# Kernel tuning notes

Hardware: AMD Instinct MI355X
Metric: run time of the kernel (lower is better)

The kernel has to match this reference:

```python
import jax, jax.numpy as jnp
import numpy as np

N_ACTIONS = 4
HIDDEN = 32

def setup_inputs() -> dict:
    key = jax.random.key(0)
    ks = jax.random.split(key, 8)
    B, T = 2048, 1024
    prev_actions_onehot = jax.random.uniform(ks[0], (B, T, N_ACTIONS), dtype=jnp.float32)
    prev_rewards = jax.random.normal(ks[1], (B, T, 1), dtype=jnp.float32)
    in_dim = N_ACTIONS + 1
    s_ih = 1.0 / np.sqrt(HIDDEN)
    W_ih = jax.random.uniform(ks[2], (HIDDEN, in_dim), jnp.float32, -s_ih, s_ih)
    W_hh = jax.random.uniform(ks[3], (HIDDEN, HIDDEN), jnp.float32, -s_ih, s_ih)
    b_ih = jax.random.uniform(ks[4], (HIDDEN,), jnp.float32, -s_ih, s_ih)
    b_hh = jax.random.uniform(ks[5], (HIDDEN,), jnp.float32, -s_ih, s_ih)
    W_ro = jax.random.uniform(ks[6], (N_ACTIONS, HIDDEN), jnp.float32, -s_ih, s_ih)
    b_ro = jax.random.uniform(ks[7], (N_ACTIONS,), jnp.float32, -s_ih, s_ih)
    return {
        'prev_actions_onehot': prev_actions_onehot,
        'prev_rewards': prev_rewards,
        'W_ih': W_ih, 'W_hh': W_hh, 'b_ih': b_ih, 'b_hh': b_hh,
        'W_ro': W_ro, 'b_ro': b_ro,
    }

def reference(prev_actions_onehot, prev_rewards, W_ih, W_hh, b_ih, b_hh, W_ro, b_ro):
    # x_seq: [B, T, n_actions+1]
    x_seq = jnp.concatenate([prev_actions_onehot, prev_rewards], axis=-1)
    B = x_seq.shape[0]
    # Precompute the input projection for all steps (parallel): [B, T, H]
    x_proj = jnp.einsum('bti,hi->bth', x_seq, W_ih) + b_ih + b_hh
    h0 = jnp.zeros((B, HIDDEN), dtype=x_seq.dtype)

    def step(h, xp_t):
        # xp_t: [B, H] (already contains x@W_ih^T + b_ih + b_hh)
        h_new = jnp.tanh(xp_t + h @ W_hh.T)
        return h_new, h_new

    # scan over time: move T to leading axis
    h_T, hs = jax.lax.scan(step, h0, jnp.swapaxes(x_proj, 0, 1))
    hs = jnp.swapaxes(hs, 0, 1)  # [B, T, H]
    logits_seq = jnp.einsum('bth,ah->bta', hs, W_ro) + b_ro  # [B, T, n_actions]
    return logits_seq, h_T
```

## Files before the change

kernel.cpp:

```cpp
#include <hip/hip_runtime.h>

#define H 32
#define GPB 8

__device__ __forceinline__ float fast_tanh(float x) {
    float e = __builtin_amdgcn_exp2f(x * 2.8853900817779268f);
    float r = __builtin_amdgcn_rcpf(e + 1.0f);
    return fmaf(-2.0f, r, 1.0f);
}

__global__ __launch_bounds__(256, 1) void rnn_fused(
    const float* __restrict__ onehot,
    const float* __restrict__ rewards,
    const float* __restrict__ W_ih,
    const float* __restrict__ W_hh,
    const float* __restrict__ b_ih,
    const float* __restrict__ b_hh,
    const float* __restrict__ W_ro,
    const float* __restrict__ b_ro,
    float* __restrict__ out_logits,
    float* __restrict__ out_hT,
    int T)
{
    const int tid = threadIdx.x;
    const int j = tid & 31;
    const int g = tid >> 5;
    const int b = blockIdx.x * GPB + g;

    __shared__ __align__(16) float hx[GPB][36];

    float whh[H];
#pragma unroll
    for (int k = 0; k < 8; ++k) {
        float4 w = *(const float4*)(W_hh + j * H + 4 * k);
        whh[4*k+0] = w.x; whh[4*k+1] = w.y; whh[4*k+2] = w.z; whh[4*k+3] = w.w;
    }
    const int a = j & 3;
    float wro[H];
#pragma unroll
    for (int k = 0; k < 8; ++k) {
        float4 w = *(const float4*)(W_ro + a * H + 4 * k);
        wro[4*k+0] = w.x; wro[4*k+1] = w.y; wro[4*k+2] = w.z; wro[4*k+3] = w.w;
    }
    const float wih0 = W_ih[j*5+0], wih1 = W_ih[j*5+1], wih2 = W_ih[j*5+2],
                wih3 = W_ih[j*5+3], wih4 = W_ih[j*5+4];
    const float bias = b_ih[j] + b_hh[j];
    const float bro  = b_ro[a];

    const float* oh_ptr = onehot  + (size_t)b * T * 4;
    const float* rw_ptr = rewards + (size_t)b * T;
    float*       lg_ptr = out_logits + (size_t)b * T * 4;

    float4 oh0 = *(const float4*)(oh_ptr + 0);
    float4 oh1 = *(const float4*)(oh_ptr + 4);
    float4 oh2 = *(const float4*)(oh_ptr + 8);
    float4 oh3 = *(const float4*)(oh_ptr + 12);
    float4 rw  = *(const float4*)(rw_ptr);

    float hj = 0.0f;
    float hA[H], hB[H];

    auto readout = [&](const float (&hv)[H], int t) {
        float l0 = 0.f, l1 = 0.f, l2 = 0.f, l3 = 0.f;
#pragma unroll
        for (int k = 0; k < 8; ++k) {
            l0 = fmaf(hv[4*k+0], wro[4*k+0], l0);
            l1 = fmaf(hv[4*k+1], wro[4*k+1], l1);
            l2 = fmaf(hv[4*k+2], wro[4*k+2], l2);
            l3 = fmaf(hv[4*k+3], wro[4*k+3], l3);
        }
        float lg = ((l0 + l1) + (l2 + l3)) + bro;
        if (j < 4) lg_ptr[(size_t)t * 4 + j] = lg;
    };

    auto step = [&](float (&cur)[H], const float (&prv)[H], float xp, int t) {
        hx[g][j] = hj;
#pragma unroll
        for (int k = 0; k < 8; ++k) {
            float4 v = *(const float4*)(&hx[g][4 * k]);
            cur[4*k+0] = v.x; cur[4*k+1] = v.y;
            cur[4*k+2] = v.z; cur[4*k+3] = v.w;
        }
        if (t >= 2) readout(prv, t - 2);
        float a0 = xp, a1 = 0.f, a2 = 0.f, a3 = 0.f;
#pragma unroll
        for (int k = 0; k < 8; ++k) {
            a0 = fmaf(cur[4*k+0], whh[4*k+0], a0);
            a1 = fmaf(cur[4*k+1], whh[4*k+1], a1);
            a2 = fmaf(cur[4*k+2], whh[4*k+2], a2);
            a3 = fmaf(cur[4*k+3], whh[4*k+3], a3);
        }
        hj = fast_tanh((a0 + a1) + (a2 + a3));
    };

    for (int tb = 0; tb < T; tb += 4) {
        float xp0 = fmaf(oh0.x,wih0, fmaf(oh0.y,wih1, fmaf(oh0.z,wih2, fmaf(oh0.w,wih3, fmaf(rw.x,wih4, bias)))));
        float xp1 = fmaf(oh1.x,wih0, fmaf(oh1.y,wih1, fmaf(oh1.z,wih2, fmaf(oh1.w,wih3, fmaf(rw.y,wih4, bias)))));
        float xp2 = fmaf(oh2.x,wih0, fmaf(oh2.y,wih1, fmaf(oh2.z,wih2, fmaf(oh2.w,wih3, fmaf(rw.z,wih4, bias)))));
        float xp3 = fmaf(oh3.x,wih0, fmaf(oh3.y,wih1, fmaf(oh3.z,wih2, fmaf(oh3.w,wih3, fmaf(rw.w,wih4, bias)))));

        if (tb + 4 < T) {
            oh0 = *(const float4*)(oh_ptr + (size_t)(tb + 4) * 4);
            oh1 = *(const float4*)(oh_ptr + (size_t)(tb + 5) * 4);
            oh2 = *(const float4*)(oh_ptr + (size_t)(tb + 6) * 4);
            oh3 = *(const float4*)(oh_ptr + (size_t)(tb + 7) * 4);
            rw  = *(const float4*)(rw_ptr + tb + 4);
        }

        step(hA, hB, xp0, tb + 0);
        step(hB, hA, xp1, tb + 1);
        step(hA, hB, xp2, tb + 2);
        step(hB, hA, xp3, tb + 3);
    }

    readout(hB, T - 2);
    hx[g][j] = hj;
#pragma unroll
    for (int k = 0; k < 8; ++k) {
        float4 v = *(const float4*)(&hx[g][4 * k]);
        hA[4*k+0] = v.x; hA[4*k+1] = v.y; hA[4*k+2] = v.z; hA[4*k+3] = v.w;
    }
    readout(hA, T - 1);
    out_hT[(size_t)b * H + j] = hj;
}

extern "C" void kernel_launch(void* const* d_in, const int* in_sizes, int n_in,
                              void* d_out, int out_size, void* d_ws, size_t ws_size,
                              hipStream_t stream) {
    const float* onehot  = (const float*)d_in[0];
    const float* rewards = (const float*)d_in[1];
    const float* W_ih    = (const float*)d_in[2];
    const float* W_hh    = (const float*)d_in[3];
    const float* b_ih    = (const float*)d_in[4];
    const float* b_hh    = (const float*)d_in[5];
    const float* W_ro    = (const float*)d_in[6];
    const float* b_ro    = (const float*)d_in[7];

    const int T = 1024;
    const int B = in_sizes[1] / T;

    float* out_logits = (float*)d_out;
    float* out_hT     = (float*)d_out + (size_t)B * T * 4;

    dim3 block(256);
    dim3 grid(B / GPB);
    rnn_fused<<<grid, block, 0, stream>>>(onehot, rewards, W_ih, W_hh,
                                          b_ih, b_hh, W_ro, b_ro,
                                          out_logits, out_hT, T);
}
```

Measured before the change: 362.3 us.

## Distribute hidden state across lane quads and use DPP FMAs for recurrence

Each lane now reads only 8 of the 32 hidden values from LDS (two float4s instead of eight). The full 32-element dot product is formed with v_fmac_f32_dpp quad_perm broadcasts that pull the other lanes' slices. The readout is spread across lanes: each lane computes a 4-term partial sum, the partials are reduced with DPP row shifts, and one lane per group of 8 writes the logit. The first iteration is peeled to drop the per-step t>=2 check. This cuts LDS read traffic and register pressure on the serial critical path, but relies on inline asm DPP semantics and on the lane-mapping being correct.

```diff
diff --git a/kernel.cpp b/kernel.cpp
--- a/kernel.cpp
+++ b/kernel.cpp
@@ -2,12 +2,29 @@
 
 #define H 32
 #define GPB 8
+#define PITCH 48
 
 __device__ __forceinline__ float fast_tanh(float x) {
     float e = __builtin_amdgcn_exp2f(x * 2.8853900817779268f);
     float r = __builtin_amdgcn_rcpf(e + 1.0f);
     return fmaf(-2.0f, r, 1.0f);
 }
+
+#define QFMA(acc, p, w, q) \
+    asm("v_fmac_f32_dpp %0, %1, %2 quad_perm:[" #q "," #q "," #q "," #q "] row_mask:0xf bank_mask:0xf" \
+        : "+v"(acc) : "v"(p), "v"(w))
+
+#define CH8(acc, q) \
+    QFMA(acc, pN[0], whh[8*q+0], q); QFMA(acc, pN[1], whh[8*q+1], q); \
+    QFMA(acc, pN[2], whh[8*q+2], q); QFMA(acc, pN[3], whh[8*q+3], q); \
+    QFMA(acc, pN[4], whh[8*q+4], q); QFMA(acc, pN[5], whh[8*q+5], q); \
+    QFMA(acc, pN[6], whh[8*q+6], q); QFMA(acc, pN[7], whh[8*q+7], q)
+
+#define DPPMOV(x, ctrl) \
+    __int_as_float(__builtin_amdgcn_update_dpp(0, __float_as_int(x), (ctrl), 0xf, 0xf, true))
+#define ROW_SHR1 0x111
+#define ROW_SHR2 0x112
+#define ROW_SHR4 0x114
 
 __global__ __launch_bounds__(256, 1) void rnn_fused(
     const float* __restrict__ onehot,
@@ -23,11 +40,18 @@
     int T)
 {
     const int tid = threadIdx.x;
-    const int j = tid & 31;
-    const int g = tid >> 5;
-    const int b = blockIdx.x * GPB + g;
+    const int j   = tid & 31;
+    const int g   = tid >> 5;
+    const int b   = blockIdx.x * GPB + g;
+    const int qp  = j & 3;
+    const int r   = j >> 3;
+    const bool hi = ((j >> 2) & 1) != 0;
+    const bool writer = (j & 7) == 7;
 
-    __shared__ __align__(16) float hx[GPB][36];
+    __shared__ __align__(16) float hx[GPB * PITCH];
+    float* lds_wr = &hx[g * PITCH + j];
+    const float4* lds_rd0 = (const float4*)&hx[g * PITCH + qp * 8];
+    const float4* lds_rd1 = lds_rd0 + 1;
 
     float whh[H];
 #pragma unroll
@@ -35,17 +59,11 @@
         float4 w = *(const float4*)(W_hh + j * H + 4 * k);
         whh[4*k+0] = w.x; whh[4*k+1] = w.y; whh[4*k+2] = w.z; whh[4*k+3] = w.w;
     }
-    const int a = j & 3;
-    float wro[H];
-#pragma unroll
-    for (int k = 0; k < 8; ++k) {
-        float4 w = *(const float4*)(W_ro + a * H + 4 * k);
-        wro[4*k+0] = w.x; wro[4*k+1] = w.y; wro[4*k+2] = w.z; wro[4*k+3] = w.w;
-    }
     const float wih0 = W_ih[j*5+0], wih1 = W_ih[j*5+1], wih2 = W_ih[j*5+2],
                 wih3 = W_ih[j*5+3], wih4 = W_ih[j*5+4];
     const float bias = b_ih[j] + b_hh[j];
-    const float bro  = b_ro[a];
+    const float4 wr4 = *(const float4*)(W_ro + r * H + qp * 8 + (hi ? 4 : 0));
+    const float bro = b_ro[r];
 
     const float* oh_ptr = onehot  + (size_t)b * T * 4;
     const float* rw_ptr = rewards + (size_t)b * T;
@@ -58,47 +76,56 @@
     float4 rw  = *(const float4*)(rw_ptr);
 
     float hj = 0.0f;
-    float hA[H], hB[H];
+    float pA[8], pB[8];
 
-    auto readout = [&](const float (&hv)[H], int t) {
-        float l0 = 0.f, l1 = 0.f, l2 = 0.f, l3 = 0.f;
-#pragma unroll
-        for (int k = 0; k < 8; ++k) {
-            l0 = fmaf(hv[4*k+0], wro[4*k+0], l0);
-            l1 = fmaf(hv[4*k+1], wro[4*k+1], l1);
-            l2 = fmaf(hv[4*k+2], wro[4*k+2], l2);
-            l3 = fmaf(hv[4*k+3], wro[4*k+3], l3);
-        }
-        float lg = ((l0 + l1) + (l2 + l3)) + bro;
-        if (j < 4) lg_ptr[(size_t)t * 4 + j] = lg;
+    auto readout = [&](const float (&p)[8], int t) {
+        float s0 = hi ? p[4] : p[0];
+        float s1 = hi ? p[5] : p[1];
+        float s2 = hi ? p[6] : p[2];
+        float s3 = hi ? p[7] : p[3];
+        float s = fmaf(s3, wr4.w, fmaf(s2, wr4.z, fmaf(s1, wr4.y, s0 * wr4.x)));
+        s += DPPMOV(s, ROW_SHR1);
+        s += DPPMOV(s, ROW_SHR2);
+        s += DPPMOV(s, ROW_SHR4);
+        if (writer) lg_ptr[(size_t)t * 4 + r] = s + bro;
     };
 
-    auto step = [&](float (&cur)[H], const float (&prv)[H], float xp, int t) {
-        hx[g][j] = hj;
-#pragma unroll
-        for (int k = 0; k < 8; ++k) {
-            float4 v = *(const float4*)(&hx[g][4 * k]);
-            cur[4*k+0] = v.x; cur[4*k+1] = v.y;
-            cur[4*k+2] = v.z; cur[4*k+3] = v.w;
-        }
-        if (t >= 2) readout(prv, t - 2);
+    auto step = [&](float (&pN)[8], const float (&pO)[8], float xp, int t, bool ro) {
+        *lds_wr = hj;
+        float4 v0 = *lds_rd0;
+        float4 v1 = *lds_rd1;
+        pN[0]=v0.x; pN[1]=v0.y; pN[2]=v0.z; pN[3]=v0.w;
+        pN[4]=v1.x; pN[5]=v1.y; pN[6]=v1.z; pN[7]=v1.w;
+        if (ro) readout(pO, t - 2);
         float a0 = xp, a1 = 0.f, a2 = 0.f, a3 = 0.f;
-#pragma unroll
-        for (int k = 0; k < 8; ++k) {
-            a0 = fmaf(cur[4*k+0], whh[4*k+0], a0);
-            a1 = fmaf(cur[4*k+1], whh[4*k+1], a1);
-            a2 = fmaf(cur[4*k+2], whh[4*k+2], a2);
-            a3 = fmaf(cur[4*k+3], whh[4*k+3], a3);
-        }
+        CH8(a0, 0);
+        CH8(a1, 1);
+        CH8(a2, 2);
+        CH8(a3, 3);
         hj = fast_tanh((a0 + a1) + (a2 + a3));
     };
 
-    for (int tb = 0; tb < T; tb += 4) {
+    {
         float xp0 = fmaf(oh0.x,wih0, fmaf(oh0.y,wih1, fmaf(oh0.z,wih2, fmaf(oh0.w,wih3, fmaf(rw.x,wih4, bias)))));
         float xp1 = fmaf(oh1.x,wih0, fmaf(oh1.y,wih1, fmaf(oh1.z,wih2, fmaf(oh1.w,wih3, fmaf(rw.y,wih4, bias)))));
         float xp2 = fmaf(oh2.x,wih0, fmaf(oh2.y,wih1, fmaf(oh2.z,wih2, fmaf(oh2.w,wih3, fmaf(rw.z,wih4, bias)))));
         float xp3 = fmaf(oh3.x,wih0, fmaf(oh3.y,wih1, fmaf(oh3.z,wih2, fmaf(oh3.w,wih3, fmaf(rw.w,wih4, bias)))));
+        oh0 = *(const float4*)(oh_ptr + 16);
+        oh1 = *(const float4*)(oh_ptr + 20);
+        oh2 = *(const float4*)(oh_ptr + 24);
+        oh3 = *(const float4*)(oh_ptr + 28);
+        rw  = *(const float4*)(rw_ptr + 4);
+        step(pA, pB, xp0, 0, false);
+        step(pB, pA, xp1, 1, false);
+        step(pA, pB, xp2, 2, true);
+        step(pB, pA, xp3, 3, true);
+    }
 
+    for (int tb = 4; tb < T; tb += 4) {
+        float xp0 = fmaf(oh0.x,wih0, fmaf(oh0.y,wih1, fmaf(oh0.z,wih2, fmaf(oh0.w,wih3, fmaf(rw.x,wih4, bias)))));
+        float xp1 = fmaf(oh1.x,wih0, fmaf(oh1.y,wih1, fmaf(oh1.z,wih2, fmaf(oh1.w,wih3, fmaf(rw.y,wih4, bias)))));
+        float xp2 = fmaf(oh2.x,wih0, fmaf(oh2.y,wih1, fmaf(oh2.z,wih2, fmaf(oh2.w,wih3, fmaf(rw.z,wih4, bias)))));
+        float xp3 = fmaf(oh3.x,wih0, fmaf(oh3.y,wih1, fmaf(oh3.z,wih2, fmaf(oh3.w,wih3, fmaf(rw.w,wih4, bias)))));
         if (tb + 4 < T) {
             oh0 = *(const float4*)(oh_ptr + (size_t)(tb + 4) * 4);
             oh1 = *(const float4*)(oh_ptr + (size_t)(tb + 5) * 4);
@@ -106,22 +133,23 @@
             oh3 = *(const float4*)(oh_ptr + (size_t)(tb + 7) * 4);
             rw  = *(const float4*)(rw_ptr + tb + 4);
         }
-
-        step(hA, hB, xp0, tb + 0);
-        step(hB, hA, xp1, tb + 1);
-        step(hA, hB, xp2, tb + 2);
-        step(hB, hA, xp3, tb + 3);
+        step(pA, pB, xp0, tb + 0, true);
+        step(pB, pA, xp1, tb + 1, true);
+        step(pA, pB, xp2, tb + 2, true);
+        step(pB, pA, xp3, tb + 3, true);
     }
 
-    readout(hB, T - 2);
-    hx[g][j] = hj;
-#pragma unroll
-    for (int k = 0; k < 8; ++k) {
-        float4 v = *(const float4*)(&hx[g][4 * k]);
-        hA[4*k+0] = v.x; hA[4*k+1] = v.y; hA[4*k+2] = v.z; hA[4*k+3] = v.w;
+    readout(pB, T - 2);
+    *lds_wr = hj;
+    {
+        float4 v0 = *lds_rd0;
+        float4 v1 = *lds_rd1;
+        pA[0]=v0.x; pA[1]=v0.y; pA[2]=v0.z; pA[3]=v0.w;
+        pA[4]=v1.x; pA[5]=v1.y; pA[6]=v1.z; pA[7]=v1.w;
     }
-    readout(hA, T - 1);
+    readout(pA, T - 1);
     out_hT[(size_t)b * H + j] = hj;
+
 }
 
 extern "C" void kernel_launch(void* const* d_in, const int* in_sizes, int n_in,
```

Measured after the change: 322.2 us. 11.1% less time.

## Replace LDS hidden-state broadcast with DPP row rotations and swizzle

Applied to the files above, without the earlier changes.

The per-step shared-memory write and read-back of the hidden vector is replaced by in-register exchange. Each step uses 15 DPP row-rotate ops within 16-lane rows plus one ds_swizzle across the two halves of the 32-lane group. The W_hh and W_ro weights are pre-permuted per lane to match the rotation order. The readout is fused into the same rotation pass, so logits for t-1 come out with the recurrence FMAs, and the explicit hA/hB arrays go away. The risk is that the recurrence now waits on a serial chain of DPP ops each step, and this relies on the DPP row semantics being correct for wave64.

```diff
diff --git a/kernel.cpp b/kernel.cpp
--- a/kernel.cpp
+++ b/kernel.cpp
@@ -8,6 +8,24 @@
     float r = __builtin_amdgcn_rcpf(e + 1.0f);
     return fmaf(-2.0f, r, 1.0f);
 }
+
+template<int K>
+__device__ __forceinline__ float rorK(float v) {
+    return __int_as_float(__builtin_amdgcn_update_dpp(
+        __float_as_int(v), __float_as_int(v), 0x120 | K, 0xf, 0xf, false));
+}
+
+#define PHK(K, V, W, R) { float tK = rorK<K>(V); \
+    aAcc[K & 1] = fmaf(tK, W[K], aAcc[K & 1]); \
+    rAcc[K & 1] = fmaf(tK, R[K], rAcc[K & 1]); }
+
+#define PHASE(V, W, R) \
+    aAcc[0] = fmaf(V, W[0], aAcc[0]); rAcc[0] = fmaf(V, R[0], rAcc[0]); \
+    PHK(1,V,W,R)  PHK(2,V,W,R)  PHK(3,V,W,R)  PHK(4,V,W,R)  PHK(5,V,W,R) \
+    PHK(6,V,W,R)  PHK(7,V,W,R)  PHK(8,V,W,R)  PHK(9,V,W,R)  PHK(10,V,W,R) \
+    PHK(11,V,W,R) PHK(12,V,W,R) PHK(13,V,W,R) PHK(14,V,W,R) PHK(15,V,W,R)
+
+#define SWIZ_XOR16 0x401F
 
 __global__ __launch_bounds__(256, 1) void rnn_fused(
     const float* __restrict__ onehot,
@@ -23,28 +41,25 @@
     int T)
 {
     const int tid = threadIdx.x;
-    const int j = tid & 31;
+    const int u = tid & 31;
     const int g = tid >> 5;
     const int b = blockIdx.x * GPB + g;
+    const int i = u & 15;
+    const int r = u >> 4;
+    const int a = u & 3;
 
-    __shared__ __align__(16) float hx[GPB][36];
-
-    float whh[H];
+    float wA[16], wB[16], roA[16], roB[16];
 #pragma unroll
-    for (int k = 0; k < 8; ++k) {
-        float4 w = *(const float4*)(W_hh + j * H + 4 * k);
-        whh[4*k+0] = w.x; whh[4*k+1] = w.y; whh[4*k+2] = w.z; whh[4*k+3] = w.w;
+    for (int k = 0; k < 16; ++k) {
+        int col = (i - k) & 15;
+        wA[k]  = W_hh[u * H + 16 * r       + col];
+        wB[k]  = W_hh[u * H + 16 * (1 - r) + col];
+        roA[k] = W_ro[a * H + 16 * r       + col];
+        roB[k] = W_ro[a * H + 16 * (1 - r) + col];
     }
-    const int a = j & 3;
-    float wro[H];
-#pragma unroll
-    for (int k = 0; k < 8; ++k) {
-        float4 w = *(const float4*)(W_ro + a * H + 4 * k);
-        wro[4*k+0] = w.x; wro[4*k+1] = w.y; wro[4*k+2] = w.z; wro[4*k+3] = w.w;
-    }
-    const float wih0 = W_ih[j*5+0], wih1 = W_ih[j*5+1], wih2 = W_ih[j*5+2],
-                wih3 = W_ih[j*5+3], wih4 = W_ih[j*5+4];
-    const float bias = b_ih[j] + b_hh[j];
+    const float wih0 = W_ih[u*5+0], wih1 = W_ih[u*5+1], wih2 = W_ih[u*5+2],
+                wih3 = W_ih[u*5+3], wih4 = W_ih[u*5+4];
+    const float bias = b_ih[u] + b_hh[u];
     const float bro  = b_ro[a];
 
     const float* oh_ptr = onehot  + (size_t)b * T * 4;
@@ -58,47 +73,40 @@
     float4 rw  = *(const float4*)(rw_ptr);
 
     float hj = 0.0f;
-    float hA[H], hB[H];
 
-    auto readout = [&](const float (&hv)[H], int t) {
-        float l0 = 0.f, l1 = 0.f, l2 = 0.f, l3 = 0.f;
-#pragma unroll
-        for (int k = 0; k < 8; ++k) {
-            l0 = fmaf(hv[4*k+0], wro[4*k+0], l0);
-            l1 = fmaf(hv[4*k+1], wro[4*k+1], l1);
-            l2 = fmaf(hv[4*k+2], wro[4*k+2], l2);
-            l3 = fmaf(hv[4*k+3], wro[4*k+3], l3);
-        }
-        float lg = ((l0 + l1) + (l2 + l3)) + bro;
-        if (j < 4) lg_ptr[(size_t)t * 4 + j] = lg;
+    auto step = [&](float xp, int tm1, bool wr) {
+        int mi = __builtin_amdgcn_ds_swizzle(__float_as_int(hj), SWIZ_XOR16);
+        float aAcc[2] = {xp, 0.f};
+        float rAcc[2] = {0.f, 0.f};
+        PHASE(hj, wA, roA);
+        float m = __int_as_float(mi);
+        PHASE(m, wB, roB);
+        hj = fast_tanh(aAcc[0] + aAcc[1]);
+        if (wr && u < 4)
+            lg_ptr[(size_t)tm1 * 4 + u] = (rAcc[0] + rAcc[1]) + bro;
     };
 
-    auto step = [&](float (&cur)[H], const float (&prv)[H], float xp, int t) {
-        hx[g][j] = hj;
-#pragma unroll
-        for (int k = 0; k < 8; ++k) {
-            float4 v = *(const float4*)(&hx[g][4 * k]);
-            cur[4*k+0] = v.x; cur[4*k+1] = v.y;
-            cur[4*k+2] = v.z; cur[4*k+3] = v.w;
-        }
-        if (t >= 2) readout(prv, t - 2);
-        float a0 = xp, a1 = 0.f, a2 = 0.f, a3 = 0.f;
-#pragma unroll
-        for (int k = 0; k < 8; ++k) {
-            a0 = fmaf(cur[4*k+0], whh[4*k+0], a0);
-            a1 = fmaf(cur[4*k+1], whh[4*k+1], a1);
-            a2 = fmaf(cur[4*k+2], whh[4*k+2], a2);
-            a3 = fmaf(cur[4*k+3], whh[4*k+3], a3);
-        }
-        hj = fast_tanh((a0 + a1) + (a2 + a3));
-    };
-
-    for (int tb = 0; tb < T; tb += 4) {
+    {
         float xp0 = fmaf(oh0.x,wih0, fmaf(oh0.y,wih1, fmaf(oh0.z,wih2, fmaf(oh0.w,wih3, fmaf(rw.x,wih4, bias)))));
         float xp1 = fmaf(oh1.x,wih0, fmaf(oh1.y,wih1, fmaf(oh1.z,wih2, fmaf(oh1.w,wih3, fmaf(rw.y,wih4, bias)))));
         float xp2 = fmaf(oh2.x,wih0, fmaf(oh2.y,wih1, fmaf(oh2.z,wih2, fmaf(oh2.w,wih3, fmaf(rw.z,wih4, bias)))));
         float xp3 = fmaf(oh3.x,wih0, fmaf(oh3.y,wih1, fmaf(oh3.z,wih2, fmaf(oh3.w,wih3, fmaf(rw.w,wih4, bias)))));
+        oh0 = *(const float4*)(oh_ptr + 16);
+        oh1 = *(const float4*)(oh_ptr + 20);
+        oh2 = *(const float4*)(oh_ptr + 24);
+        oh3 = *(const float4*)(oh_ptr + 28);
+        rw  = *(const float4*)(rw_ptr + 4);
+        step(xp0, -1, false);
+        step(xp1,  0, true);
+        step(xp2,  1, true);
+        step(xp3,  2, true);
+    }
 
+    for (int tb = 4; tb < T; tb += 4) {
+        float xp0 = fmaf(oh0.x,wih0, fmaf(oh0.y,wih1, fmaf(oh0.z,wih2, fmaf(oh0.w,wih3, fmaf(rw.x,wih4, bias)))));
+        float xp1 = fmaf(oh1.x,wih0, fmaf(oh1.y,wih1, fmaf(oh1.z,wih2, fmaf(oh1.w,wih3, fmaf(rw.y,wih4, bias)))));
+        float xp2 = fmaf(oh2.x,wih0, fmaf(oh2.y,wih1, fmaf(oh2.z,wih2, fmaf(oh2.w,wih3, fmaf(rw.z,wih4, bias)))));
+        float xp3 = fmaf(oh3.x,wih0, fmaf(oh3.y,wih1, fmaf(oh3.z,wih2, fmaf(oh3.w,wih3, fmaf(rw.w,wih4, bias)))));
         if (tb + 4 < T) {
             oh0 = *(const float4*)(oh_ptr + (size_t)(tb + 4) * 4);
             oh1 = *(const float4*)(oh_ptr + (size_t)(tb + 5) * 4);
@@ -106,22 +114,25 @@
             oh3 = *(const float4*)(oh_ptr + (size_t)(tb + 7) * 4);
             rw  = *(const float4*)(rw_ptr + tb + 4);
         }
-
-        step(hA, hB, xp0, tb + 0);
-        step(hB, hA, xp1, tb + 1);
-        step(hA, hB, xp2, tb + 2);
-        step(hB, hA, xp3, tb + 3);
+        step(xp0, tb - 1, true);
+        step(xp1, tb + 0, true);
+        step(xp2, tb + 1, true);
+        step(xp3, tb + 2, true);
     }
 
-    readout(hB, T - 2);
-    hx[g][j] = hj;
-#pragma unroll
-    for (int k = 0; k < 8; ++k) {
-        float4 v = *(const float4*)(&hx[g][4 * k]);
-        hA[4*k+0] = v.x; hA[4*k+1] = v.y; hA[4*k+2] = v.z; hA[4*k+3] = v.w;
+    {
+        int mi = __builtin_amdgcn_ds_swizzle(__float_as_int(hj), SWIZ_XOR16);
+        float aAcc[2] = {0.f, 0.f};
+        float rAcc[2] = {0.f, 0.f};
+        PHASE(hj, wA, roA);
+        float m = __int_as_float(mi);
+        PHASE(m, wB, roB);
+        (void)aAcc;
+        if (u < 4)
+            lg_ptr[(size_t)(T - 1) * 4 + u] = (rAcc[0] + rAcc[1]) + bro;
     }
-    readout(hA, T - 1);
-    out_hT[(size_t)b * H + j] = hj;
+    out_hT[(size_t)b * H + u] = hj;
+
 }
 
 extern "C" void kernel_launch(void* const* d_in, const int* in_sizes, int n_in,
```

New measurement: 393.8 us. 8.7% more time.

## Split hidden matvec across half-waves with DPP FMAs and bpermute broadcasts, interleaving two sequences

Applied to the files above, without the earlier changes.

Each 64-lane wave now handles two batch sequences. For each sequence, the K dimension of the W_hh matvec is split across the two 32-lane halves and the partial sums are exchanged with ds_bpermute. The hidden state is stored as the sigmoid-form r = 1/(1+e^{2y}), with tanh = 1 - 2r folded into the weights (-2*W) and constant terms (rsum, roconst). The h broadcast uses bpermute plus DPP quad_perm FMAs instead of LDS stores and loads. The readout uses DPP row shifts for its reduction, and interleaving the two independent recurrences is meant to hide dependency latency, at the cost of more cross-lane traffic and reliance on inline assembly.

```diff
diff --git a/kernel.cpp b/kernel.cpp
--- a/kernel.cpp
+++ b/kernel.cpp
@@ -1,13 +1,22 @@
 #include <hip/hip_runtime.h>
 
-#define H 32
-#define GPB 8
-
-__device__ __forceinline__ float fast_tanh(float x) {
-    float e = __builtin_amdgcn_exp2f(x * 2.8853900817779268f);
-    float r = __builtin_amdgcn_rcpf(e + 1.0f);
-    return fmaf(-2.0f, r, 1.0f);
-}
+#define KK 2.8853900817779268f
+
+#define QFMA(acc, p, w, q) \
+    asm("v_fmac_f32_dpp %0, %1, %2 quad_perm:[" #q "," #q "," #q "," #q "] row_mask:0xf bank_mask:0xf" \
+        : "+v"(acc) : "v"(p), "v"(w))
+
+#define Q4(acc, p, w2, q) \
+    QFMA(acc, p[0], w2[4*q+0], q); QFMA(acc, p[1], w2[4*q+1], q); \
+    QFMA(acc, p[2], w2[4*q+2], q); QFMA(acc, p[3], w2[4*q+3], q)
+
+#define DPPMOV(x, ctrl) \
+    __int_as_float(__builtin_amdgcn_update_dpp(0, __float_as_int(x), (ctrl), 0xf, 0xf, true))
+#define ROW_SHR1 0x111
+#define ROW_SHR2 0x112
+#define ROW_SHR4 0x114
+
+#define BPERM(idx, v) __builtin_amdgcn_ds_bpermute((idx), (v))
 
 __global__ __launch_bounds__(256, 1) void rnn_fused(
     const float* __restrict__ onehot,
@@ -22,106 +31,178 @@
     float* __restrict__ out_hT,
     int T)
 {
-    const int tid = threadIdx.x;
-    const int j = tid & 31;
-    const int g = tid >> 5;
-    const int b = blockIdx.x * GPB + g;
-
-    __shared__ __align__(16) float hx[GPB][36];
-
-    float whh[H];
+    const int tid  = threadIdx.x;
+    const int l    = tid & 63;
+    const int wv   = tid >> 6;
+    const int s    = l >> 5;
+    const int u    = l & 31;
+    const int qp   = l & 3;
+    const int ridx = u >> 3;
+    const bool oddq = ((u >> 2) & 1) != 0;
+    const bool writer = (l < 32) && ((u & 7) == 7);
+
+    const int bA = blockIdx.x * 8 + 2 * wv;
+    const int bB = bA + 1;
+
+    const int gib = (48 * s + 4 * qp) << 2;
+    const int lx  = (l ^ 32) << 2;
+
+    float w2[16];
+    float rsum = 0.f;
 #pragma unroll
-    for (int k = 0; k < 8; ++k) {
-        float4 w = *(const float4*)(W_hh + j * H + 4 * k);
-        whh[4*k+0] = w.x; whh[4*k+1] = w.y; whh[4*k+2] = w.z; whh[4*k+3] = w.w;
-    }
-    const int a = j & 3;
-    float wro[H];
+    for (int k4 = 0; k4 < 4; ++k4) {
+        float4 wq = *(const float4*)(W_hh + u * 32 + 16 * s + 4 * k4);
+        rsum += (wq.x + wq.y) + (wq.z + wq.w);
+        w2[4*k4+0] = -2.f * wq.x; w2[4*k4+1] = -2.f * wq.y;
+        w2[4*k4+2] = -2.f * wq.z; w2[4*k4+3] = -2.f * wq.w;
+    }
+    const float wih0 = W_ih[u*5+0], wih1 = W_ih[u*5+1], wih2 = W_ih[u*5+2],
+                wih3 = W_ih[u*5+3], wih4 = W_ih[u*5+4];
+    const float bias = b_ih[u] + b_hh[u];
+
+    float wro2[4];
+    {
+        float4 wq = *(const float4*)(W_ro + ridx * 32 + 16 * s + 4 * qp);
+        wro2[0] = oddq ? 0.f : -2.f * wq.x;
+        wro2[1] = oddq ? 0.f : -2.f * wq.y;
+        wro2[2] = oddq ? 0.f : -2.f * wq.z;
+        wro2[3] = oddq ? 0.f : -2.f * wq.w;
+    }
+    float roconst = b_ro[ridx];
 #pragma unroll
-    for (int k = 0; k < 8; ++k) {
-        float4 w = *(const float4*)(W_ro + a * H + 4 * k);
-        wro[4*k+0] = w.x; wro[4*k+1] = w.y; wro[4*k+2] = w.z; wro[4*k+3] = w.w;
-    }
-    const float wih0 = W_ih[j*5+0], wih1 = W_ih[j*5+1], wih2 = W_ih[j*5+2],
-                wih3 = W_ih[j*5+3], wih4 = W_ih[j*5+4];
-    const float bias = b_ih[j] + b_hh[j];
-    const float bro  = b_ro[a];
-
-    const float* oh_ptr = onehot  + (size_t)b * T * 4;
-    const float* rw_ptr = rewards + (size_t)b * T;
-    float*       lg_ptr = out_logits + (size_t)b * T * 4;
-
-    float4 oh0 = *(const float4*)(oh_ptr + 0);
-    float4 oh1 = *(const float4*)(oh_ptr + 4);
-    float4 oh2 = *(const float4*)(oh_ptr + 8);
-    float4 oh3 = *(const float4*)(oh_ptr + 12);
-    float4 rw  = *(const float4*)(rw_ptr);
-
-    float hj = 0.0f;
-    float hA[H], hB[H];
-
-    auto readout = [&](const float (&hv)[H], int t) {
-        float l0 = 0.f, l1 = 0.f, l2 = 0.f, l3 = 0.f;
-#pragma unroll
-        for (int k = 0; k < 8; ++k) {
-            l0 = fmaf(hv[4*k+0], wro[4*k+0], l0);
-            l1 = fmaf(hv[4*k+1], wro[4*k+1], l1);
-            l2 = fmaf(hv[4*k+2], wro[4*k+2], l2);
-            l3 = fmaf(hv[4*k+3], wro[4*k+3], l3);
-        }
-        float lg = ((l0 + l1) + (l2 + l3)) + bro;
-        if (j < 4) lg_ptr[(size_t)t * 4 + j] = lg;
+    for (int k4 = 0; k4 < 8; ++k4) {
+        float4 t4 = *(const float4*)(W_ro + ridx * 32 + 4 * k4);
+        roconst += (t4.x + t4.y) + (t4.z + t4.w);
+    }
+
+    const float* ohpA = onehot  + (size_t)bA * T * 4;
+    const float* ohpB = onehot  + (size_t)bB * T * 4;
+    const float* rwpA = rewards + (size_t)bA * T;
+    const float* rwpB = rewards + (size_t)bB * T;
+    float*       lgpA = out_logits + (size_t)bA * T * 4;
+    float*       lgpB = out_logits + (size_t)bB * T * 4;
+
+    float4 A0 = *(const float4*)(ohpA + 0), A1 = *(const float4*)(ohpA + 4);
+    float4 A2 = *(const float4*)(ohpA + 8), A3 = *(const float4*)(ohpA + 12);
+    float4 Ar = *(const float4*)(rwpA);
+    float4 B0 = *(const float4*)(ohpB + 0), B1 = *(const float4*)(ohpB + 4);
+    float4 B2 = *(const float4*)(ohpB + 8), B3 = *(const float4*)(ohpB + 12);
+    float4 Br = *(const float4*)(rwpB);
+
+    float rA = 0.5f, rB = 0.5f;
+    float pA[4] = {0.5f, 0.5f, 0.5f, 0.5f};
+    float pB[4] = {0.5f, 0.5f, 0.5f, 0.5f};
+
+    auto macro = [&](float xa, float xb, int tm1, bool ro) {
+        float xaE = s ? 0.f : xa;
+        float xbE = s ? 0.f : xb;
+        float a0 = xaE + rsum, a1 = 0.f;
+        Q4(a0, pA, w2, 0); Q4(a0, pA, w2, 1);
+        Q4(a1, pA, w2, 2); Q4(a1, pA, w2, 3);
+        float partA = a0 + a1;
+        int XA = BPERM(lx, __float_as_int(partA));
+        float rpA = fmaf(pA[3], wro2[3], fmaf(pA[2], wro2[2],
+                    fmaf(pA[1], wro2[1], pA[0] * wro2[0])));
+        rpA += DPPMOV(rpA, ROW_SHR1);
+        rpA += DPPMOV(rpA, ROW_SHR2);
+        rpA += DPPMOV(rpA, ROW_SHR4);
+        int XRA = BPERM(lx, __float_as_int(rpA));
+        float b0 = xbE + rsum, b1 = 0.f;
+        Q4(b0, pB, w2, 0); Q4(b0, pB, w2, 1);
+        Q4(b1, pB, w2, 2); Q4(b1, pB, w2, 3);
+        float partB = b0 + b1;
+        int XB = BPERM(lx, __float_as_int(partB));
+        float rpB = fmaf(pB[3], wro2[3], fmaf(pB[2], wro2[2],
+                    fmaf(pB[1], wro2[1], pB[0] * wro2[0])));
+        rpB += DPPMOV(rpB, ROW_SHR1);
+        rpB += DPPMOV(rpB, ROW_SHR2);
+        rpB += DPPMOV(rpB, ROW_SHR4);
+        int XRB = BPERM(lx, __float_as_int(rpB));
+        float yA = partA + __int_as_float(XA);
+        rA = __builtin_amdgcn_rcpf(__builtin_amdgcn_exp2f(KK * yA) + 1.0f);
+        {
+            int hb = __float_as_int(rA);
+            pA[0] = __int_as_float(BPERM(gib +  0, hb));
+            pA[1] = __int_as_float(BPERM(gib +  4, hb));
+            pA[2] = __int_as_float(BPERM(gib +  8, hb));
+            pA[3] = __int_as_float(BPERM(gib + 12, hb));
+        }
+        if (ro && writer)
+            lgpA[(size_t)tm1 * 4 + ridx] = (rpA + __int_as_float(XRA)) + roconst;
+        float yB = partB + __int_as_float(XB);
+        rB = __builtin_amdgcn_rcpf(__builtin_amdgcn_exp2f(KK * yB) + 1.0f);
+        {
+            int hb = __float_as_int(rB);
+            pB[0] = __int_as_float(BPERM(gib +  0, hb));
+            pB[1] = __int_as_float(BPERM(gib +  4, hb));
+            pB[2] = __int_as_float(BPERM(gib +  8, hb));
+            pB[3] = __int_as_float(BPERM(gib + 12, hb));
+        }
+        if (ro && writer)
+            lgpB[(size_t)tm1 * 4 + ridx] = (rpB + __int_as_float(XRB)) + roconst;
     };
 
-    auto step = [&](float (&cur)[H], const float (&prv)[H], float xp, int t) {
-        hx[g][j] = hj;
-#pragma unroll
-        for (int k = 0; k < 8; ++k) {
-            float4 v = *(const float4*)(&hx[g][4 * k]);
-            cur[4*k+0] = v.x; cur[4*k+1] = v.y;
-            cur[4*k+2] = v.z; cur[4*k+3] = v.w;
-        }
-        if (t >= 2) readout(prv, t - 2);
-        float a0 = xp, a1 = 0.f, a2 = 0.f, a3 = 0.f;
-#pragma unroll
-        for (int k = 0; k < 8; ++k) {
-            a0 = fmaf(cur[4*k+0], whh[4*k+0], a0);
-            a1 = fmaf(cur[4*k+1], whh[4*k+1], a1);
-            a2 = fmaf(cur[4*k+2], whh[4*k+2], a2);
-            a3 = fmaf(cur[4*k+3], whh[4*k+3], a3);
-        }
-        hj = fast_tanh((a0 + a1) + (a2 + a3));
-    };
-
-    for (int tb = 0; tb < T; tb += 4) {
-        float xp0 = fmaf(oh0.x,wih0, fmaf(oh0.y,wih1, fmaf(oh0.z,wih2, fmaf(oh0.w,wih3, fmaf(rw.x,wih4, bias)))));
-        float xp1 = fmaf(oh1.x,wih0, fmaf(oh1.y,wih1, fmaf(oh1.z,wih2, fmaf(oh1.w,wih3, fmaf(rw.y,wih4, bias)))));
-        float xp2 = fmaf(oh2.x,wih0, fmaf(oh2.y,wih1, fmaf(oh2.z,wih2, fmaf(oh2.w,wih3, fmaf(rw.z,wih4, bias)))));
-        float xp3 = fmaf(oh3.x,wih0, fmaf(oh3.y,wih1, fmaf(oh3.z,wih2, fmaf(oh3.w,wih3, fmaf(rw.w,wih4, bias)))));
-
+#define XP(oh, rwc) fmaf((oh).x, wih0, fmaf((oh).y, wih1, fmaf((oh).z, wih2, \
+                     fmaf((oh).w, wih3, fmaf((rwc), wih4, bias)))))
+
+    {
+        float xa0 = XP(A0, Ar.x), xa1 = XP(A1, Ar.y), xa2 = XP(A2, Ar.z), xa3 = XP(A3, Ar.w);
+        float xb0 = XP(B0, Br.x), xb1 = XP(B1, Br.y), xb2 = XP(B2, Br.z), xb3 = XP(B3, Br.w);
+        A0 = *(const float4*)(ohpA + 16); A1 = *(const float4*)(ohpA + 20);
+        A2 = *(const float4*)(ohpA + 24); A3 = *(const float4*)(ohpA + 28);
+        Ar = *(const float4*)(rwpA + 4);
+        B0 = *(const float4*)(ohpB + 16); B1 = *(const float4*)(ohpB + 20);
+        B2 = *(const float4*)(ohpB + 24); B3 = *(const float4*)(ohpB + 28);
+        Br = *(const float4*)(rwpB + 4);
+        macro(xa0, xb0, -1, false);
+        macro(xa1, xb1,  0, true);
+        macro(xa2, xb2,  1, true);
+        macro(xa3, xb3,  2, true);
+    }
+
+    for (int tb = 4; tb < T; tb += 4) {
+        float xa0 = XP(A0, Ar.x), xa1 = XP(A1, Ar.y), xa2 = XP(A2, Ar.z), xa3 = XP(A3, Ar.w);
+        float xb0 = XP(B0, Br.x), xb1 = XP(B1, Br.y), xb2 = XP(B2, Br.z), xb3 = XP(B3, Br.w);
         if (tb + 4 < T) {
-            oh0 = *(const float4*)(oh_ptr + (size_t)(tb + 4) * 4);
-            oh1 = *(const float4*)(oh_ptr + (size_t)(tb + 5) * 4);
-            oh2 = *(const float4*)(oh_ptr + (size_t)(tb + 6) * 4);
-            oh3 = *(const float4*)(oh_ptr + (size_t)(tb + 7) * 4);
-            rw  = *(const float4*)(rw_ptr + tb + 4);
-        }
-
-        step(hA, hB, xp0, tb + 0);
-        step(hB, hA, xp1, tb + 1);
-        step(hA, hB, xp2, tb + 2);
-        step(hB, hA, xp3, tb + 3);
-    }
-
-    readout(hB, T - 2);
-    hx[g][j] = hj;
-#pragma unroll
-    for (int k = 0; k < 8; ++k) {
-        float4 v = *(const float4*)(&hx[g][4 * k]);
-        hA[4*k+0] = v.x; hA[4*k+1] = v.y; hA[4*k+2] = v.z; hA[4*k+3] = v.w;
-    }
-    readout(hA, T - 1);
-    out_hT[(size_t)b * H + j] = hj;
+            A0 = *(const float4*)(ohpA + (size_t)(tb + 4) * 4);
+            A1 = *(const float4*)(ohpA + (size_t)(tb + 5) * 4);
+            A2 = *(const float4*)(ohpA + (size_t)(tb + 6) * 4);
+            A3 = *(const float4*)(ohpA + (size_t)(tb + 7) * 4);
+            Ar = *(const float4*)(rwpA + tb + 4);
+            B0 = *(const float4*)(ohpB + (size_t)(tb + 4) * 4);
+            B1 = *(const float4*)(ohpB + (size_t)(tb + 5) * 4);
+            B2 = *(const float4*)(ohpB + (size_t)(tb + 6) * 4);
+            B3 = *(const float4*)(ohpB + (size_t)(tb + 7) * 4);
+            Br = *(const float4*)(rwpB + tb + 4);
+        }
+        macro(xa0, xb0, tb - 1, true);
+        macro(xa1, xb1, tb + 0, true);
+        macro(xa2, xb2, tb + 1, true);
+        macro(xa3, xb3, tb + 2, true);
+    }
+
+    {
+        float rpA = fmaf(pA[3], wro2[3], fmaf(pA[2], wro2[2],
+                    fmaf(pA[1], wro2[1], pA[0] * wro2[0])));
+        rpA += DPPMOV(rpA, ROW_SHR1);
+        rpA += DPPMOV(rpA, ROW_SHR2);
+        rpA += DPPMOV(rpA, ROW_SHR4);
+        int XRA = BPERM(lx, __float_as_int(rpA));
+        float rpB = fmaf(pB[3], wro2[3], fmaf(pB[2], wro2[2],
+                    fmaf(pB[1], wro2[1], pB[0] * wro2[0])));
+        rpB += DPPMOV(rpB, ROW_SHR1);
+        rpB += DPPMOV(rpB, ROW_SHR2);
+        rpB += DPPMOV(rpB, ROW_SHR4);
+        int XRB = BPERM(lx, __float_as_int(rpB));
+        if (writer) {
+            lgpA[(size_t)(T - 1) * 4 + ridx] = (rpA + __int_as_float(XRA)) + roconst;
+            lgpB[(size_t)(T - 1) * 4 + ridx] = (rpB + __int_as_float(XRB)) + roconst;
+        }
+    }
+    if (l < 32) {
+        out_hT[(size_t)bA * 32 + u] = fmaf(-2.f, rA, 1.f);
+        out_hT[(size_t)bB * 32 + u] = fmaf(-2.f, rB, 1.f);
+    }
 }
 
 extern "C" void kernel_launch(void* const* d_in, const int* in_sizes, int n_in,
@@ -143,7 +224,7 @@
     float* out_hT     = (float*)d_out + (size_t)B * T * 4;
 
     dim3 block(256);
-    dim3 grid(B / GPB);
+    dim3 grid(B / 8);
     rnn_fused<<<grid, block, 0, stream>>>(onehot, rewards, W_ih, W_hh,
                                           b_ih, b_hh, W_ro, b_ro,
                                           out_logits, out_hT, T);
```

Result: slower. 437.3 us (+20.7%).
